# Kernel tuning notes

Hardware: AMD Instinct MI355X
Metric: run time of the kernel (lower is better)

The kernel has to match this reference:

```python
import jax, jax.numpy as jnp
import numpy as np

B, N, S, K = 8, 4096, 1024, 16
C_IN, C_OUT = 128, 256
BN_EPS = 1e-5


def setup_inputs() -> dict:
    key = jax.random.key(0)
    ks = jax.random.split(key, 20)
    sc = 0.02
    p = {
        'xyz': jax.random.normal(ks[0], (B, N, 3), jnp.float32),
        'points': jax.random.normal(ks[1], (B, N, C_IN), jnp.float32),
        'wq': jax.random.normal(ks[2], (C_IN, C_OUT), jnp.float32) * sc,
        'wk': jax.random.normal(ks[3], (C_IN, C_OUT), jnp.float32) * sc,
        'wv': jax.random.normal(ks[4], (C_IN, C_OUT), jnp.float32) * sc,
        'dw1': jax.random.normal(ks[5], (3, C_OUT), jnp.float32) * sc,
        'db1': jnp.zeros((C_OUT,), jnp.float32),
        'dw2': jax.random.normal(ks[6], (C_OUT, C_OUT), jnp.float32) * sc,
        'db2': jnp.zeros((C_OUT,), jnp.float32),
        'gw1': jax.random.normal(ks[7], (C_OUT, C_OUT), jnp.float32) * sc,
        'gb1': jnp.zeros((C_OUT,), jnp.float32),
        'gw2': jax.random.normal(ks[8], (C_OUT, C_OUT), jnp.float32) * sc,
        'gb2': jnp.zeros((C_OUT,), jnp.float32),
        'lw': jax.random.normal(ks[9], (C_OUT, C_OUT), jnp.float32) * sc,
        'lb': jnp.zeros((C_OUT,), jnp.float32),
        'bn_g': jnp.ones((C_OUT,), jnp.float32),
        'bn_b': jnp.zeros((C_OUT,), jnp.float32),
    }
    return p


def _fps(xyz, npoint):
    # xyz: [N,3] -> farthest point sample indices [npoint] (deterministic start at 0,
    # matching torch impl with fixed seed semantics)
    n = xyz.shape[0]
    def step(carry, _):
        dist, far = carry
        centroid = xyz[far]                      # [3]
        d = jnp.sum((xyz - centroid) ** 2, -1)   # [N]
        dist = jnp.minimum(dist, d)
        return (dist, jnp.argmax(dist).astype(jnp.int32)), far
    init = (jnp.full((n,), 1e10, xyz.dtype), jnp.int32(0))
    _, idx = jax.lax.scan(step, init, None, length=npoint)
    return idx  # [npoint]


def _mlp2(x, w1, b1, w2, b2):
    return jax.nn.relu(x @ w1 + b1) @ w2 + b2


def reference(xyz, points, wq, wk, wv, dw1, db1, dw2, db2,
              gw1, gb1, gw2, gb2, lw, lb, bn_g, bn_b):
    # --- sample_and_group (FPS + KNN, knn=True) ---
    fps_idx = jax.vmap(lambda x: _fps(x, S))(xyz)                 # [B,S]
    new_xyz = jnp.take_along_axis(xyz, fps_idx[..., None], 1)     # [B,S,3]
    # squared distances sampled->all: [B,S,N]
    d2 = (jnp.sum(new_xyz**2, -1)[:, :, None]
          - 2.0 * jnp.einsum('bsc,bnc->bsn', new_xyz, xyz)
          + jnp.sum(xyz**2, -1)[:, None, :])
    knn_idx = jax.lax.top_k(-d2, K)[1]                            # [B,S,K]
    gather = jax.vmap(lambda a, i: a[i])
    knn_xyz = gather(xyz, knn_idx)                                # [B,S,K,3]
    knn_xyz_norm = knn_xyz - new_xyz[:, :, None]                  # centered coords
    knn_points = gather(points, knn_idx)                          # [B,S,K,C_in]
    sampled_points = jnp.take_along_axis(points, fps_idx[..., None], 1)  # [B,S,C_in]

    # --- vector attention ---
    q = sampled_points @ wq                                       # [B,S,C_out]
    k = knn_points @ wk                                           # [B,S,K,C_out]
    v = knn_points @ wv                                           # [B,S,K,C_out]
    pos_enc = _mlp2(knn_xyz_norm, dw1, db1, dw2, db2)             # [B,S,K,C_out]
    att = _mlp2(q[:, :, None] - k + pos_enc, gw1, gb1, gw2, gb2)  # [B,S,K,C_out]
    att = jax.nn.softmax(att / np.sqrt(C_OUT).astype(np.float32), axis=-2)
    res = jnp.einsum('bmnf,bmnf->bmf', att, v + pos_enc)          # [B,S,C_out]

    # --- fc_last + BatchNorm1d (training-mode batch stats, biased var) + ReLU ---
    res = res @ lw + lb
    mean = jnp.mean(res, axis=(0, 1))
    var = jnp.var(res, axis=(0, 1))
    res = bn_g * (res - mean) * jax.lax.rsqrt(var + BN_EPS) + bn_b
    res = jax.nn.relu(res)
    return new_xyz, res
```

## Files before the change

### kernel.cpp

```cpp
#include <hip/hip_runtime.h>

typedef unsigned long long ull;
typedef __attribute__((ext_vector_type(8))) short bf16x8;
typedef __attribute__((ext_vector_type(4))) float f32x4;

__device__ __forceinline__ unsigned short bf16b(float x){
    unsigned u = __float_as_uint(x);
    unsigned r = (u + 0x7FFFu + ((u >> 16) & 1u)) >> 16;
    return (unsigned short)r;
}
__device__ __forceinline__ float b2f(unsigned short u){
    return __uint_as_float(((unsigned)u) << 16);
}
__device__ __forceinline__ void st4(unsigned short* p, f32x4 v){
    ull pk = (ull)bf16b(v[0]) | (((ull)bf16b(v[1])) << 16)
           | (((ull)bf16b(v[2])) << 32) | (((ull)bf16b(v[3])) << 48);
    *(ull*)p = pk;
}
__device__ __forceinline__ f32x4 ld4(const unsigned short* p){
    ull pk = *(const ull*)p;
    f32x4 v;
    v[0] = b2f((unsigned short)pk);
    v[1] = b2f((unsigned short)(pk >> 16));
    v[2] = b2f((unsigned short)(pk >> 32));
    v[3] = b2f((unsigned short)(pk >> 48));
    return v;
}

#define DPPMAX(k, ctrl) do { \
    unsigned _lo = (unsigned)(k), _hi = (unsigned)((k) >> 32); \
    unsigned _l2 = (unsigned)__builtin_amdgcn_update_dpp((int)_lo, (int)_lo, (ctrl), 0xF, 0xF, false); \
    unsigned _h2 = (unsigned)__builtin_amdgcn_update_dpp((int)_hi, (int)_hi, (ctrl), 0xF, 0xF, false); \
    ull _k2 = (((ull)_h2) << 32) | _l2; \
    if (_k2 > (k)) (k) = _k2; \
} while (0)
#define DPPMIN(k, ctrl) do { \
    unsigned _lo = (unsigned)(k), _hi = (unsigned)((k) >> 32); \
    unsigned _l2 = (unsigned)__builtin_amdgcn_update_dpp((int)_lo, (int)_lo, (ctrl), 0xF, 0xF, false); \
    unsigned _h2 = (unsigned)__builtin_amdgcn_update_dpp((int)_hi, (int)_hi, (ctrl), 0xF, 0xF, false); \
    ull _k2 = (((ull)_h2) << 32) | _l2; \
    if (_k2 < (k)) (k) = _k2; \
} while (0)

template<int KT>
__device__ __forceinline__ int swz(int r, int c){
    return r * (KT * 32) + ((((c >> 3) + r) & (KT * 4 - 1)) << 3) + (c & 7);
}

template<int KT>
__device__ __forceinline__ void gemmT(const unsigned short* __restrict__ Wt,
                                      const unsigned short* __restrict__ Blds,
                                      int ch0, int lane, f32x4 acc[4][4])
{
    int i = lane & 15, q = lane >> 4;
#pragma unroll
    for (int kt = 0; kt < KT; kt++){
        int k0 = kt * 32 + q * 8;
        bf16x8 bfr[4], afr[4];
#pragma unroll
        for (int nt = 0; nt < 4; nt++)
            bfr[nt] = *(const bf16x8*)(Blds + swz<KT>(nt * 16 + i, k0));
#pragma unroll
        for (int mt = 0; mt < 4; mt++)
            afr[mt] = *(const bf16x8*)(Wt + (size_t)(ch0 + mt * 16 + i) * (KT * 32) + k0);
#pragma unroll
        for (int mt = 0; mt < 4; mt++)
#pragma unroll
            for (int nt = 0; nt < 4; nt++)
                acc[mt][nt] = __builtin_amdgcn_mfma_f32_16x16x32_bf16(afr[mt], bfr[nt], acc[mt][nt], 0, 0, 0);
    }
}

#define ZERO44(A) do { _Pragma("unroll") for (int _m = 0; _m < 4; _m++) \
    { _Pragma("unroll") for (int _n = 0; _n < 4; _n++) { A[_m][_n][0]=0.f;A[_m][_n][1]=0.f;A[_m][_n][2]=0.f;A[_m][_n][3]=0.f; } } } while(0)

#define CTRL_AUX   (8 << 4)

__device__ __forceinline__ int ald_sys(const int* p){
    return __hip_atomic_load(p, __ATOMIC_RELAXED, __HIP_MEMORY_SCOPE_SYSTEM);
}
__device__ __forceinline__ void ast_sys(int* p, int v){
    __hip_atomic_store(p, v, __ATOMIC_RELAXED, __HIP_MEMORY_SCOPE_SYSTEM);
}

__device__ __forceinline__ void knn_one(int t2, int G, float qx, float qy, float qz,
        const float* __restrict__ xyz,
        int* __restrict__ knn_idx, ull* kslot )
{
    int b = G >> 10;
    int lane = t2 & 63, wvi = t2 >> 6;
    float qq = qx * qx + qy * qy + qz * qz;
    unsigned fb[16];
#pragma unroll
    for (int j = 0; j < 16; j++){
        int p = t2 + (j << 8);
        const float* s = xyz + ((size_t)b * 4096 + p) * 3;
        float x = s[0], y = s[1], z = s[2];
        float d2 = qq - 2.f * (qx * x + qy * y + qz * z) + (x * x + y * y + z * z);
        unsigned bb = __float_as_uint(d2);
        fb[j] = (bb & 0x80000000u) ? ~bb : (bb | 0x80000000u);
    }
    ull lk = ~0ull;
#pragma unroll
    for (int j = 0; j < 16; j++){
        ull key = (((ull)fb[j]) << 32) | (unsigned)(t2 + (j << 8));
        if (key < lk) lk = key;
    }
    int par = 0;
    for (int r = 0; r < 16; r++){
        ull k = lk;
        DPPMIN(k, 0xB1); DPPMIN(k, 0x4E); DPPMIN(k, 0x141);
        DPPMIN(k, 0x140); DPPMIN(k, 0x142); DPPMIN(k, 0x143);
        if (lane == 63) kslot[par * 4 + wvi] = k;
        __syncthreads();
        ull s0 = kslot[par * 4 + 0], s1 = kslot[par * 4 + 1];
        ull s2 = kslot[par * 4 + 2], s3 = kslot[par * 4 + 3];
        ull ga = s0 < s1 ? s0 : s1;
        ull gb = s2 < s3 ? s2 : s3;
        ull g  = ga < gb ? ga : gb;
        int p = (int)(unsigned)g;
        if (t2 == (p & 255)){
            knn_idx[(size_t)G * 16 + r] = p;
            int jw = p >> 8;
            lk = ~0ull;
#pragma unroll
            for (int j = 0; j < 16; j++){
                if (j == jw) fb[j] = 0xFFFFFFFFu;
                ull key = (((ull)fb[j]) << 32) | (unsigned)(t2 + (j << 8));
                if (key < lk) lk = key;
            }
        }
        par ^= 1;
    }
}

__device__ void attn_unit(int t, char* base, int G0, const float* nxL4,
    const unsigned short* __restrict__ pts16,
    const float* __restrict__ xyz,
    const int* __restrict__ knn_idx, const float* __restrict__ qbuf,
    const unsigned short* __restrict__ wkT, const unsigned short* __restrict__ wvT,
    const unsigned short* __restrict__ dw2T, const unsigned short* __restrict__ gw1T,
    const unsigned short* __restrict__ gw2T,
    const float* __restrict__ dw1, const float* __restrict__ db1,
    const float* __restrict__ db2, const float* __restrict__ gb1, const float* __restrict__ gb2,
    unsigned short* __restrict__ resY)
{
    unsigned short* bufA = (unsigned short*)base;
    unsigned short* bufU = (unsigned short*)(base + 32768);
    int lane = t & 63, wave = t >> 6;
    int i = lane & 15, q = lane >> 4;
    int ch0 = wave * 64;
    unsigned short* ptsA = bufU;
    float* dw1s  = (float*)(bufU + 8192);
    float* db1s  = (float*)(bufU + 9728);
    float* xyznS = (float*)(bufU + 10240);
    int*   idxs  = (int*)  (bufU + 10624);

    if (t < 64) idxs[t] = knn_idx[G0 * 16 + t];
    dw1s[t] = dw1[t]; dw1s[256 + t] = dw1[256 + t]; dw1s[512 + t] = dw1[512 + t];
    db1s[t] = db1[t];
    __syncthreads();

    if (t < 64){
        int G = G0 + (t >> 4); int bb = G >> 10; int p = idxs[t];
        const float* xp = xyz + ((size_t)bb * 4096 + p) * 3;
        const float* nz = nxL4 + (t >> 4) * 3;
        xyznS[t * 3 + 0] = xp[0] - nz[0];
        xyznS[t * 3 + 1] = xp[1] - nz[1];
        xyznS[t * 3 + 2] = xp[2] - nz[2];
    }
    {
        int r = t >> 2, seg = t & 3;
        int G = G0 + (r >> 4); int bb = G >> 10; int p = idxs[r];
        const uint4* src = (const uint4*)(pts16 + ((size_t)bb * 4096 + p) * 128 + seg * 32);
#pragma unroll
        for (int j = 0; j < 4; j++){
            uint4 v = src[j];
            *(uint4*)(ptsA + swz<4>(r, seg * 32 + j * 8)) = v;
        }
    }
    __syncthreads();

    {
        int r = lane;
        int o0 = wave * 64;
        float x = xyznS[r * 3], y = xyznS[r * 3 + 1], z = xyznS[r * 3 + 2];
#pragma unroll
        for (int j = 0; j < 64; j += 4){
            int o = o0 + j;
            f32x4 v;
#pragma unroll
            for (int e = 0; e < 4; e++)
                v[e] = fmaxf(db1s[o + e] + x * dw1s[o + e] + y * dw1s[256 + o + e] + z * dw1s[512 + o + e], 0.f);
            st4(bufA + swz<8>(r, o), v);
        }
    }
    __syncthreads();

    f32x4 accP[4][4]; ZERO44(accP);
    gemmT<8>(dw2T, bufA, ch0, lane, accP);
#pragma unroll
    for (int mt = 0; mt < 4; mt++){
        f32x4 d2v = *(const f32x4*)(db2 + ch0 + mt * 16 + q * 4);
#pragma unroll
        for (int nt = 0; nt < 4; nt++) accP[mt][nt] += d2v;
    }
    f32x4 accK[4][4]; ZERO44(accK);
    gemmT<4>(wkT, ptsA, ch0, lane, accK);
    __syncthreads();

#pragma unroll
    for (int mt = 0; mt < 4; mt++){
        int c = ch0 + mt * 16 + q * 4;
#pragma unroll
        for (int nt = 0; nt < 4; nt++){
            int r = nt * 16 + i;
            f32x4 qv = *(const f32x4*)(qbuf + (size_t)(G0 + nt) * 256 + c);
            f32x4 tv = qv - accK[mt][nt] + accP[mt][nt];
            st4(bufA + swz<8>(r, c), tv);
        }
    }
    f32x4 accV[4][4]; ZERO44(accV);
    gemmT<4>(wvT, ptsA, ch0, lane, accV);
    __syncthreads();

#pragma unroll
    for (int mt = 0; mt < 4; mt++){
        int c = ch0 + mt * 16 + q * 4;
#pragma unroll
        for (int nt = 0; nt < 4; nt++){
            int r = nt * 16 + i;
            f32x4 uv = accV[mt][nt] + accP[mt][nt];
            st4(bufU + swz<8>(r, c), uv);
        }
    }
    f32x4 acc1[4][4]; ZERO44(acc1);
    gemmT<8>(gw1T, bufA, ch0, lane, acc1);
    __syncthreads();

#pragma unroll
    for (int mt = 0; mt < 4; mt++){
        int c = ch0 + mt * 16 + q * 4;
        f32x4 g1v = *(const f32x4*)(gb1 + c);
#pragma unroll
        for (int nt = 0; nt < 4; nt++){
            int r = nt * 16 + i;
            f32x4 av = acc1[mt][nt] + g1v;
#pragma unroll
            for (int e = 0; e < 4; e++) av[e] = fmaxf(av[e], 0.f);
            st4(bufA + swz<8>(r, c), av);
        }
    }
    __syncthreads();

    f32x4 acc2[4][4]; ZERO44(acc2);
    gemmT<8>(gw2T, bufA, ch0, lane, acc2);
    __syncthreads();

#pragma unroll
    for (int mt = 0; mt < 4; mt++){
        int c = ch0 + mt * 16 + q * 4;
        f32x4 g2v = *(const f32x4*)(gb2 + c);
#pragma unroll
        for (int nt = 0; nt < 4; nt++){
            int r = nt * 16 + i;
            f32x4 ev;
#pragma unroll
            for (int e = 0; e < 4; e++) ev[e] = __expf((acc2[mt][nt][e] + g2v[e]) * 0.0625f);
            st4(bufA + swz<8>(r, c), ev);
        }
    }
    __syncthreads();

    {
        int g = t >> 6, c4 = (t & 63) * 4;
        f32x4 num; num[0]=0.f;num[1]=0.f;num[2]=0.f;num[3]=0.f;
        f32x4 den = num;
#pragma unroll
        for (int rr = 0; rr < 16; rr++){
            int r = g * 16 + rr;
            f32x4 e4 = ld4(bufA + swz<8>(r, c4));
            f32x4 u4 = ld4(bufU + swz<8>(r, c4));
            num += e4 * u4;
            den += e4;
        }
        f32x4 rv = num / den;
        st4(resY + (size_t)(G0 + g) * 256 + c4, rv);
    }
}

__device__ void do_chunk(int t, int c, char* SM,
    const float* __restrict__ xyz, const float* __restrict__ nxyz,
    const float* __restrict__ points, const float* __restrict__ wqT,
    const int* __restrict__ fps_idx, int* __restrict__ knn_idx, float* __restrict__ qbuf,
    const unsigned short* __restrict__ pts16,
    const unsigned short* __restrict__ wkT, const unsigned short* __restrict__ wvT,
    const unsigned short* __restrict__ dw2T, const unsigned short* __restrict__ gw1T,
    const unsigned short* __restrict__ gw2T,
    const float* __restrict__ dw1, const float* __restrict__ db1,
    const float* __restrict__ db2, const float* __restrict__ gb1, const float* __restrict__ gb2,
    unsigned short* __restrict__ resY)
{
    int g0 = c * 8;
    int sub = t >> 8, t2 = t & 255;
    ull*   kslot = (ull*)(SM + 131072) + sub * 8;
    int*   fpsL  = (int*)  (SM + 131200);
    float* nxL   = (float*)(SM + 131232);
    if (t < 64){
        for (;;){
            int v = 0; bool ok = true;
            if (t < 8){
                v = ald_sys(fps_idx + g0 + t); ok = (v != -1);
            } else if (t < 32){
                v = ald_sys((const int*)nxyz + (size_t)g0 * 3 + (t - 8)); ok = (v != (int)0xFFFFFFFF);
            }
            if (__ballot(ok) == ~0ull){
                if (t < 8) fpsL[t] = v;
                else if (t < 32) ((int*)nxL)[t - 8] = v;
                break;
            }
            __builtin_amdgcn_s_sleep(8);
        }
    }
    __syncthreads();
    for (int r4 = 0; r4 < 4; r4++){
        int gl = r4 * 2 + sub;
        knn_one(t2, g0 + gl, nxL[gl * 3], nxL[gl * 3 + 1], nxL[gl * 3 + 2],
                xyz, knn_idx, kslot);
    }
    __syncthreads();
    {
        float* sp = (float*)SM;
        if (t < 256){
            int r = t >> 5, c4 = (t & 31) * 4;
            int G = g0 + r; int b = G >> 10; int p = fpsL[r];
            *(f32x4*)(sp + r * 128 + c4) = *(const f32x4*)(points + ((size_t)b * 4096 + p) * 128 + c4);
        }
        __syncthreads();
        float acc[4] = {0.f, 0.f, 0.f, 0.f};
        const float* wr = wqT + t2 * 128;
        for (int k = 0; k < 128; k += 4){
            f32x4 w = *(const f32x4*)(wr + k);
#pragma unroll
            for (int r = 0; r < 4; r++){
                const float* row = sp + (sub * 4 + r) * 128;
                acc[r] += w[0]*row[k] + w[1]*row[k+1] + w[2]*row[k+2] + w[3]*row[k+3];
            }
        }
#pragma unroll
        for (int r = 0; r < 4; r++) qbuf[(size_t)(g0 + sub * 4 + r) * 256 + t2] = acc[r];
        __syncthreads();
    }
    attn_unit(t2, SM + sub * 65536, g0 + sub * 4, nxL + sub * 12, pts16, xyz, knn_idx, qbuf,
              wkT, wvT, dw2T, gw1T, gw2T, dw1, db1, db2, gb1, gb2, resY);
    __syncthreads();
}

__global__ __launch_bounds__(256) void init_ws(int* __restrict__ ctrl,
                                               int* __restrict__ fps_idx,
                                               int* __restrict__ nxyz_i)
{
    int i = blockIdx.x * 256 + threadIdx.x;
    if (i < 256) ctrl[i] = 0;
    if (i < 8192) fps_idx[i] = -1;
    if (i < 24576) nxyz_i[i] = (int)0xFFFFFFFF;
}

__global__ __launch_bounds__(512, 2) void mega(
    const float* __restrict__ xyz, float* __restrict__ nxyz_out, int* __restrict__ fps_idx,
    const float* __restrict__ pts, unsigned short* __restrict__ pts16,
    const float* __restrict__ wq, const float* __restrict__ wk, const float* __restrict__ wv,
    const float* __restrict__ dw2, const float* __restrict__ gw1, const float* __restrict__ gw2,
    const float* __restrict__ lw,
    float* __restrict__ wqT, unsigned short* __restrict__ wkT, unsigned short* __restrict__ wvT,
    unsigned short* __restrict__ dw2T, unsigned short* __restrict__ gw1T,
    unsigned short* __restrict__ gw2T, unsigned short* __restrict__ lwT,
    float* __restrict__ stats,
    const float* __restrict__ dw1, const float* __restrict__ db1, const float* __restrict__ db2,
    const float* __restrict__ gb1, const float* __restrict__ gb2,
    int* __restrict__ knn_idx, float* __restrict__ qbuf, unsigned short* __restrict__ resY,
    int* __restrict__ ctrl)
{
    __shared__ __align__(16) char SM[132096];
    int blk = blockIdx.x, t = threadIdx.x;

    if (blk < 8){
        int b = blk;
        int lane = t & 63, wvi = t >> 6;
        float* sx = (float*)SM;
        float* sy = (float*)(SM + 16384);
        float* sz = (float*)(SM + 32768);
        ull (*slotK)[8] = (ull(*)[8])(SM + 53248);
        for (int p = t; p < 4096; p += 512){
            const float* s = xyz + ((size_t)b * 4096 + p) * 3;
            sx[p] = s[0]; sy[p] = s[1]; sz[p] = s[2];
        }
        __syncthreads();
        float px[8], py[8], pz[8], dist[8];
        unsigned nplo[8];
#pragma unroll
        for (int j = 0; j < 8; j++){
            int p = t + (j << 9);
            px[j] = sx[p]; py[j] = sy[p]; pz[j] = sz[p];
            dist[j] = 1e10f;
            nplo[j] = ~(unsigned)p;
            asm volatile("" : "+v"(px[j]), "+v"(py[j]), "+v"(pz[j]), "+v"(nplo[j]));
        }
        int myStep = 99, myD = 0;
        int* pubp = nullptr;
        if (wvi == 7){
            if (lane < 16){
                myStep = lane;
                pubp = fps_idx + b * 1024 + lane;
            } else {
                int idx = lane - 16;
                myStep = idx / 3; myD = idx - myStep * 3;
                pubp = (int*)nxyz_out + (size_t)b * 3072 + myStep * 3 + myD;
            }
        }
        unsigned hv = 0;
        int far = 0;
        float cx = sx[0], cy = sy[0], cz = sz[0];
        int par = 0;
        for (int s = 0; s < 1024; s++){
            if (wvi == 7 && (s & 15) == myStep)
                hv = (lane < 16) ? (unsigned)far
                                 : __float_as_uint(myD == 0 ? cx : (myD == 1 ? cy : cz));
            ull lb = 0;
#pragma unroll
            for (int j = 0; j < 8; j++){
                float dx = __fsub_rn(px[j], cx);
                float dy = __fsub_rn(py[j], cy);
                float dz = __fsub_rn(pz[j], cz);
                float d = __fadd_rn(__fadd_rn(__fmul_rn(dx, dx), __fmul_rn(dy, dy)), __fmul_rn(dz, dz));
                float nd = fminf(dist[j], d);
                dist[j] = nd;
                ull k2 = (((ull)__float_as_uint(nd)) << 32) | nplo[j];
                if (k2 > lb) lb = k2;
            }
            DPPMAX(lb, 0xB1); DPPMAX(lb, 0x4E); DPPMAX(lb, 0x141);
            DPPMAX(lb, 0x140); DPPMAX(lb, 0x142); DPPMAX(lb, 0x143);
            if (lane == 63) slotK[par][wvi] = lb;
            __syncthreads();
            ull k = slotK[par][lane & 7];
            DPPMAX(k, 0xB1); DPPMAX(k, 0x4E); DPPMAX(k, 0x141);
            far = (int)(~(unsigned)k);
            cx = sx[far]; cy = sy[far]; cz = sz[far];
            if (wvi == 7 && (s & 15) == 15){
                ast_sys(pubp, (int)hv);
                pubp += 16 * ((lane < 16) ? 1 : 3);
            }
            par ^= 1;
        }
        if (t == 0){ while (ald_sys(ctrl + CTRL_AUX) < 248) __builtin_amdgcn_s_sleep(16); }
        __syncthreads();
        __threadfence();
        do_chunk(t, b * 128 + 127, SM, xyz, nxyz_out, pts, wqT, fps_idx, knn_idx, qbuf,
                 pts16, wkT, wvT, dw2T, gw1T, gw2T, dw1, db1, db2, gb1, gb2, resY);
        return;
    }

    int w = blk - 8;
    for (int base = w; base < 704; base += 248){
        if (base == 0) stats[t & 511] = 0.f;
        int i = base * 512 + t;
        if (i < 32768){ int n = i >> 7, kk = i & 127; wqT[i] = wq[kk * 256 + n]; }
        else if (i < 65536){ int j = i - 32768; int n = j >> 7, kk = j & 127; wkT[j] = bf16b(wk[kk * 256 + n]); }
        else if (i < 98304){ int j = i - 65536; int n = j >> 7, kk = j & 127; wvT[j] = bf16b(wv[kk * 256 + n]); }
        else if (i < 163840){ int j = i - 98304; int n = j >> 8, kk = j & 255; dw2T[j] = bf16b(dw2[kk * 256 + n]); }
        else if (i < 229376){ int j = i - 163840; int n = j >> 8, kk = j & 255; gw1T[j] = bf16b(gw1[kk * 256 + n]); }
        else if (i < 294912){ int j = i - 229376; int n = j >> 8, kk = j & 255; gw2T[j] = bf16b(gw2[kk * 256 + n]); }
        else { int j = i - 294912; int n = j >> 8, kk = j & 255; lwT[j] = bf16b(lw[kk * 256 + n]); }
    }
    for (int base = w; base < 2048; base += 248){
        int i = (base * 512 + t) * 4;
        f32x4 v = *(const f32x4*)(pts + i);
        ull pk = (ull)bf16b(v[0]) | (((ull)bf16b(v[1])) << 16)
               | (((ull)bf16b(v[2])) << 32) | (((ull)bf16b(v[3])) << 48);
        *(ull*)(pts16 + i) = pk;
    }
    __threadfence();
    __syncthreads();
    if (t == 0){
        atomicAdd(ctrl + CTRL_AUX, 1);
        while (ald_sys(ctrl + CTRL_AUX) < 248) __builtin_amdgcn_s_sleep(16);
    }
    __syncthreads();
    __threadfence();
    for (int j = 0; j < 5; j++){
        int p = w + 248 * j;
        if (p >= 1016) break;
        int bb = p & 7, cc = p >> 3;
        do_chunk(t, bb * 128 + cc, SM, xyz, nxyz_out, pts, wqT, fps_idx, knn_idx, qbuf,
                 pts16, wkT, wvT, dw2T, gw1T, gw2T, dw1, db1, db2, gb1, gb2, resY);
    }
}

__global__ __launch_bounds__(256, 2) void z_gemm(const unsigned short* __restrict__ resY,
                                                 const unsigned short* __restrict__ lwT,
                                                 const float* __restrict__ lb,
                                                 float* __restrict__ zbuf,
                                                 float* __restrict__ stats)
{
    int t = threadIdx.x, lane = t & 63, wave = t >> 6;
    int i = lane & 15, q = lane >> 4;
    int row0 = blockIdx.x * 128;
    int ch0 = wave * 64;
    f32x4 acc[4][8];
#pragma unroll
    for (int mt = 0; mt < 4; mt++)
#pragma unroll
        for (int nt = 0; nt < 8; nt++){ acc[mt][nt][0]=0.f;acc[mt][nt][1]=0.f;acc[mt][nt][2]=0.f;acc[mt][nt][3]=0.f; }
#pragma unroll
    for (int kt = 0; kt < 8; kt++){
        int k0 = kt * 32 + q * 8;
        bf16x8 a[4], bb[8];
#pragma unroll
        for (int mt = 0; mt < 4; mt++)
            a[mt] = *(const bf16x8*)(lwT + (size_t)(ch0 + mt * 16 + i) * 256 + k0);
#pragma unroll
        for (int nt = 0; nt < 8; nt++)
            bb[nt] = *(const bf16x8*)(resY + (size_t)(row0 + nt * 16 + i) * 256 + k0);
#pragma unroll
        for (int mt = 0; mt < 4; mt++)
#pragma unroll
            for (int nt = 0; nt < 8; nt++)
                acc[mt][nt] = __builtin_amdgcn_mfma_f32_16x16x32_bf16(a[mt], bb[nt], acc[mt][nt], 0, 0, 0);
    }
    f32x4 s1[4], s2[4];
#pragma unroll
    for (int mt = 0; mt < 4; mt++){ s1[mt][0]=0.f;s1[mt][1]=0.f;s1[mt][2]=0.f;s1[mt][3]=0.f; s2[mt]=s1[mt]; }
#pragma unroll
    for (int mt = 0; mt < 4; mt++){
        int c = ch0 + mt * 16 + q * 4;
        f32x4 lb4 = *(const f32x4*)(lb + c);
#pragma unroll
        for (int nt = 0; nt < 8; nt++){
            int r = row0 + nt * 16 + i;
            f32x4 z = acc[mt][nt] + lb4;
            *(f32x4*)(zbuf + (size_t)r * 256 + c) = z;
            s1[mt] += z;
            s2[mt] += z * z;
        }
    }
    for (int m = 1; m < 16; m <<= 1){
#pragma unroll
        for (int mt = 0; mt < 4; mt++)
#pragma unroll
            for (int e = 0; e < 4; e++){
                s1[mt][e] += __shfl_xor(s1[mt][e], m);
                s2[mt][e] += __shfl_xor(s2[mt][e], m);
            }
    }
    if (i == 0){
#pragma unroll
        for (int mt = 0; mt < 4; mt++){
            int c = ch0 + mt * 16 + q * 4;
#pragma unroll
            for (int e = 0; e < 4; e++){
                atomicAdd(&stats[c + e], s1[mt][e]);
                atomicAdd(&stats[256 + c + e], s2[mt][e]);
            }
        }
    }
}

__global__ __launch_bounds__(256) void bn_kernel(const float* __restrict__ zbuf,
                                                 const float* __restrict__ stats,
                                                 const float* __restrict__ bn_g,
                                                 const float* __restrict__ bn_b,
                                                 float* __restrict__ out)
{
    int G = blockIdx.x, c = threadIdx.x;
    float mean = stats[c] * (1.f / 8192.f);
    float var = stats[256 + c] * (1.f / 8192.f) - mean * mean;
    float inv = rsqrtf(var + 1e-5f);
    float z = zbuf[(size_t)G * 256 + c];
    float y = bn_g[c] * (z - mean) * inv + bn_b[c];
    out[24576 + (size_t)G * 256 + c] = fmaxf(y, 0.f);
}

extern "C" void kernel_launch(void* const* d_in, const int* in_sizes, int n_in,
                              void* d_out, int out_size, void* d_ws, size_t ws_size,
                              hipStream_t stream)
{
    const float* xyz    = (const float*)d_in[0];
    const float* points = (const float*)d_in[1];
    const float* wq  = (const float*)d_in[2];
    const float* wk  = (const float*)d_in[3];
    const float* wv  = (const float*)d_in[4];
    const float* dw1 = (const float*)d_in[5];
    const float* db1 = (const float*)d_in[6];
    const float* dw2 = (const float*)d_in[7];
    const float* db2 = (const float*)d_in[8];
    const float* gw1 = (const float*)d_in[9];
    const float* gb1 = (const float*)d_in[10];
    const float* gw2 = (const float*)d_in[11];
    const float* gb2 = (const float*)d_in[12];
    const float* lw  = (const float*)d_in[13];
    const float* lb  = (const float*)d_in[14];
    const float* bn_g = (const float*)d_in[15];
    const float* bn_b = (const float*)d_in[16];
    float* out = (float*)d_out;

    char* ws = (char*)d_ws;
    int*            fps_idx = (int*)(ws + 0);
    int*            knn_idx = (int*)(ws + 32768);
    float*          qbuf    = (float*)(ws + 557056);
    unsigned short* pts16   = (unsigned short*)(ws + 8945664);
    unsigned short* wkT     = (unsigned short*)(ws + 17334272);
    unsigned short* wvT     = (unsigned short*)(ws + 17399808);
    unsigned short* dw2T    = (unsigned short*)(ws + 17465344);
    unsigned short* gw1T    = (unsigned short*)(ws + 17596416);
    unsigned short* gw2T    = (unsigned short*)(ws + 17727488);
    unsigned short* lwT     = (unsigned short*)(ws + 17858560);
    float*          wqT     = (float*)(ws + 17989632);
    unsigned short* resY    = (unsigned short*)(ws + 18120704);
    float*          zbuf    = (float*)(ws + 22315008);
    float*          stats   = (float*)(ws + 30703616);
    int*            ctrl    = (int*)(ws + 22315008);

    init_ws<<<96, 256, 0, stream>>>(ctrl, fps_idx, (int*)out);
    mega<<<256, 512, 0, stream>>>(xyz, out, fps_idx, points, pts16,
                                  wq, wk, wv, dw2, gw1, gw2, lw,
                                  wqT, wkT, wvT, dw2T, gw1T, gw2T, lwT, stats,
                                  dw1, db1, db2, gb1, gb2,
                                  knn_idx, qbuf, resY, ctrl);
    z_gemm<<<64, 256, 0, stream>>>(resY, lwT, lb, zbuf, stats);
    bn_kernel<<<8192, 256, 0, stream>>>(zbuf, stats, bn_g, bn_b, out);
}
```

Before: 851.5 us.

## Split tail FPS chunk into half-size pieces and fuse BN into z-GEMM

```diff
diff --git a/kernel.cpp b/kernel.cpp
--- a/kernel.cpp
+++ b/kernel.cpp
@@ -289,7 +289,8 @@
     }
 }
 
-__device__ void do_chunk(int t, int c, char* SM,
+template<int NG>
+__device__ void do_chunk(int t, int g0, char* SM,
     const float* __restrict__ xyz, const float* __restrict__ nxyz,
     const float* __restrict__ points, const float* __restrict__ wqT,
     const int* __restrict__ fps_idx, int* __restrict__ knn_idx, float* __restrict__ qbuf,
@@ -301,7 +302,6 @@
     const float* __restrict__ db2, const float* __restrict__ gb1, const float* __restrict__ gb2,
     unsigned short* __restrict__ resY)
 {
-    int g0 = c * 8;
     int sub = t >> 8, t2 = t & 255;
     ull*   kslot = (ull*)(SM + 131072) + sub * 8;
     int*   fpsL  = (int*)  (SM + 131200);
@@ -309,21 +309,21 @@
     if (t < 64){
         for (;;){
             int v = 0; bool ok = true;
-            if (t < 8){
+            if (t < NG){
                 v = ald_sys(fps_idx + g0 + t); ok = (v != -1);
-            } else if (t < 32){
-                v = ald_sys((const int*)nxyz + (size_t)g0 * 3 + (t - 8)); ok = (v != (int)0xFFFFFFFF);
+            } else if (t < 4 * NG){
+                v = ald_sys((const int*)nxyz + (size_t)g0 * 3 + (t - NG)); ok = (v != (int)0xFFFFFFFF);
             }
             if (__ballot(ok) == ~0ull){
-                if (t < 8) fpsL[t] = v;
-                else if (t < 32) ((int*)nxL)[t - 8] = v;
+                if (t < NG) fpsL[t] = v;
+                else if (t < 4 * NG) ((int*)nxL)[t - NG] = v;
                 break;
             }
             __builtin_amdgcn_s_sleep(8);
         }
     }
     __syncthreads();
-    for (int r4 = 0; r4 < 4; r4++){
+    for (int r4 = 0; r4 < NG / 2; r4++){
         int gl = r4 * 2 + sub;
         knn_one(t2, g0 + gl, nxL[gl * 3], nxL[gl * 3 + 1], nxL[gl * 3 + 2],
                 xyz, knn_idx, kslot);
@@ -331,37 +331,44 @@
     __syncthreads();
     {
         float* sp = (float*)SM;
-        if (t < 256){
+        if (t < NG * 32){
             int r = t >> 5, c4 = (t & 31) * 4;
             int G = g0 + r; int b = G >> 10; int p = fpsL[r];
             *(f32x4*)(sp + r * 128 + c4) = *(const f32x4*)(points + ((size_t)b * 4096 + p) * 128 + c4);
         }
         __syncthreads();
-        float acc[4] = {0.f, 0.f, 0.f, 0.f};
+        float acc[NG / 2];
+#pragma unroll
+        for (int r = 0; r < NG / 2; r++) acc[r] = 0.f;
         const float* wr = wqT + t2 * 128;
         for (int k = 0; k < 128; k += 4){
             f32x4 w = *(const f32x4*)(wr + k);
 #pragma unroll
-            for (int r = 0; r < 4; r++){
-                const float* row = sp + (sub * 4 + r) * 128;
+            for (int r = 0; r < NG / 2; r++){
+                const float* row = sp + (sub * (NG / 2) + r) * 128;
                 acc[r] += w[0]*row[k] + w[1]*row[k+1] + w[2]*row[k+2] + w[3]*row[k+3];
             }
         }
 #pragma unroll
-        for (int r = 0; r < 4; r++) qbuf[(size_t)(g0 + sub * 4 + r) * 256 + t2] = acc[r];
+        for (int r = 0; r < NG / 2; r++)
+            qbuf[(size_t)(g0 + sub * (NG / 2) + r) * 256 + t2] = acc[r];
         __syncthreads();
     }
-    attn_unit(t2, SM + sub * 65536, g0 + sub * 4, nxL + sub * 12, pts16, xyz, knn_idx, qbuf,
+    int aG0 = (NG == 8) ? (g0 + sub * 4) : g0;
+    const float* anx = (NG == 8) ? (nxL + sub * 12) : nxL;
+    attn_unit(t2, SM + sub * 65536, aG0, anx, pts16, xyz, knn_idx, qbuf,
               wkT, wvT, dw2T, gw1T, gw2T, dw1, db1, db2, gb1, gb2, resY);
     __syncthreads();
 }
 
 __global__ __launch_bounds__(256) void init_ws(int* __restrict__ ctrl,
                                                int* __restrict__ fps_idx,
-                                               int* __restrict__ nxyz_i)
+                                               int* __restrict__ nxyz_i,
+                                               int* __restrict__ stats_i)
 {
     int i = blockIdx.x * 256 + threadIdx.x;
     if (i < 256) ctrl[i] = 0;
+    if (i == 0) stats_i[512] = 0;
     if (i < 8192) fps_idx[i] = -1;
     if (i < 24576) nxyz_i[i] = (int)0xFFFFFFFF;
 }
@@ -455,8 +462,8 @@
         if (t == 0){ while (ald_sys(ctrl + CTRL_AUX) < 248) __builtin_amdgcn_s_sleep(16); }
         __syncthreads();
         __threadfence();
-        do_chunk(t, b * 128 + 127, SM, xyz, nxyz_out, pts, wqT, fps_idx, knn_idx, qbuf,
-                 pts16, wkT, wvT, dw2T, gw1T, gw2T, dw1, db1, db2, gb1, gb2, resY);
+        do_chunk<4>(t, b * 1024 + 1016, SM, xyz, nxyz_out, pts, wqT, fps_idx, knn_idx, qbuf,
+                    pts16, wkT, wvT, dw2T, gw1T, gw2T, dw1, db1, db2, gb1, gb2, resY);
         return;
     }
 
@@ -491,17 +498,26 @@
         int p = w + 248 * j;
         if (p >= 1016) break;
         int bb = p & 7, cc = p >> 3;
-        do_chunk(t, bb * 128 + cc, SM, xyz, nxyz_out, pts, wqT, fps_idx, knn_idx, qbuf,
-                 pts16, wkT, wvT, dw2T, gw1T, gw2T, dw1, db1, db2, gb1, gb2, resY);
-    }
-}
-
-__global__ __launch_bounds__(256, 2) void z_gemm(const unsigned short* __restrict__ resY,
-                                                 const unsigned short* __restrict__ lwT,
-                                                 const float* __restrict__ lb,
-                                                 float* __restrict__ zbuf,
-                                                 float* __restrict__ stats)
-{
+        do_chunk<8>(t, (bb * 128 + cc) * 8, SM, xyz, nxyz_out, pts, wqT, fps_idx, knn_idx, qbuf,
+                    pts16, wkT, wvT, dw2T, gw1T, gw2T, dw1, db1, db2, gb1, gb2, resY);
+    }
+    if (w >= 240){
+        int b2 = w - 240;
+        do_chunk<4>(t, b2 * 1024 + 1020, SM, xyz, nxyz_out, pts, wqT, fps_idx, knn_idx, qbuf,
+                    pts16, wkT, wvT, dw2T, gw1T, gw2T, dw1, db1, db2, gb1, gb2, resY);
+    }
+}
+
+__global__ __launch_bounds__(256, 2) void z_bn(const unsigned short* __restrict__ resY,
+                                               const unsigned short* __restrict__ lwT,
+                                               const float* __restrict__ lb,
+                                               float* __restrict__ zbuf,
+                                               float* __restrict__ stats,
+                                               const float* __restrict__ bn_g,
+                                               const float* __restrict__ bn_b,
+                                               float* __restrict__ out)
+{
+    __shared__ float mean_s[256], inv_s[256];
     int t = threadIdx.x, lane = t & 63, wave = t >> 6;
     int i = lane & 15, q = lane >> 4;
     int row0 = blockIdx.x * 128;
@@ -563,21 +579,41 @@
             }
         }
     }
-}
-
-__global__ __launch_bounds__(256) void bn_kernel(const float* __restrict__ zbuf,
-                                                 const float* __restrict__ stats,
-                                                 const float* __restrict__ bn_g,
-                                                 const float* __restrict__ bn_b,
-                                                 float* __restrict__ out)
-{
-    int G = blockIdx.x, c = threadIdx.x;
-    float mean = stats[c] * (1.f / 8192.f);
-    float var = stats[256 + c] * (1.f / 8192.f) - mean * mean;
-    float inv = rsqrtf(var + 1e-5f);
-    float z = zbuf[(size_t)G * 256 + c];
-    float y = bn_g[c] * (z - mean) * inv + bn_b[c];
-    out[24576 + (size_t)G * 256 + c] = fmaxf(y, 0.f);
+    __threadfence();
+    __syncthreads();
+    int* done = (int*)(stats + 512);
+    if (t == 0){
+        atomicAdd(done, 1);
+        while (ald_sys(done) < 64) __builtin_amdgcn_s_sleep(16);
+    }
+    __syncthreads();
+    {
+        float s1v = __int_as_float(ald_sys((const int*)stats + t));
+        float s2v = __int_as_float(ald_sys((const int*)stats + 256 + t));
+        float m = s1v * (1.f / 8192.f);
+        float var = s2v * (1.f / 8192.f) - m * m;
+        mean_s[t] = m;
+        inv_s[t] = rsqrtf(var + 1e-5f);
+    }
+    __syncthreads();
+#pragma unroll
+    for (int mt = 0; mt < 4; mt++){
+        int c = ch0 + mt * 16 + q * 4;
+        f32x4 mm = *(const f32x4*)&mean_s[c];
+        f32x4 vv = *(const f32x4*)&inv_s[c];
+        f32x4 gg = *(const f32x4*)(bn_g + c);
+        f32x4 bbv = *(const f32x4*)(bn_b + c);
+#pragma unroll
+        for (int nt = 0; nt < 8; nt++){
+            int r = row0 + nt * 16 + i;
+            f32x4 z = *(const f32x4*)(zbuf + (size_t)r * 256 + c);
+            f32x4 y;
+#pragma unroll
+            for (int e = 0; e < 4; e++)
+                y[e] = fmaxf(gg[e] * (z[e] - mm[e]) * vv[e] + bbv[e], 0.f);
+            *(f32x4*)(out + 24576 + (size_t)r * 256 + c) = y;
+        }
+    }
 }
 
 extern "C" void kernel_launch(void* const* d_in, const int* in_sizes, int n_in,
@@ -620,12 +656,11 @@
     float*          stats   = (float*)(ws + 30703616);
     int*            ctrl    = (int*)(ws + 22315008);
 
-    init_ws<<<96, 256, 0, stream>>>(ctrl, fps_idx, (int*)out);
+    init_ws<<<96, 256, 0, stream>>>(ctrl, fps_idx, (int*)out, (int*)stats);
     mega<<<256, 512, 0, stream>>>(xyz, out, fps_idx, points, pts16,
                                   wq, wk, wv, dw2, gw1, gw2, lw,
                                   wqT, wkT, wvT, dw2T, gw1T, gw2T, lwT, stats,
                                   dw1, db1, db2, gb1, gb2,
                                   knn_idx, qbuf, resY, ctrl);
-    z_gemm<<<64, 256, 0, stream>>>(resY, lwT, lb, zbuf, stats);
-    bn_kernel<<<8192, 256, 0, stream>>>(zbuf, stats, bn_g, bn_b, out);
-}
+    z_bn<<<64, 256, 0, stream>>>(resY, lwT, lb, zbuf, stats, bn_g, bn_b, out);
+}
```

After: 1.287 ms. 51.1% more time.
